# Optimization experiments

Measured on AMD Instinct MI355X. Metric: run time of the kernel, lower is better.

The kernel has to match this reference:

```python
import jax, jax.numpy as jnp
import numpy as np

EPS = 1e-6

def _rms(x, scale):
    # flax nn.RMSNorm: x / sqrt(mean(x^2)+eps) * scale, no mean subtraction
    return x * scale * jax.lax.rsqrt(jnp.mean(x * x, axis=-1, keepdims=True) + EPS)


def _forward(x, mem_k, mem_v, norm1_scale, norm2_scale,
             Wq, bq, Wk, bk, Wv, bv, Wz, bz,
             Wgz, bgz, Wgh, bgh,
             Wg1, bg1, Wg2, bg2, Wgc1, bgc1, Wgc2, bgc2,
             Awq, abq, Awk, abk, Awv, abv, Awo, abo,
             Wf1, bf1, Wf2, bf2):
    B, S, D = x.shape
    M = mem_k.shape[1]
    H = 8
    hd = D // H

    x_norm = _rms(x, norm1_scale)
    q = x_norm @ Wq + bq
    k = x_norm @ Wk + bk
    v = x_norm @ Wv + bv
    z = x_norm @ Wz + bz

    # input-dependent decay gamma in (1e-6, 1-1e-6)
    gamma_base = jax.nn.sigmoid(jax.nn.gelu(z @ Wg1 + bg1) @ Wg2 + bg2)
    gamma_mod = jax.nn.sigmoid(jax.nn.gelu(k @ Wgc1 + bgc1) @ Wgc2 + bgc2)
    gamma = jnp.clip(gamma_base * gamma_mod, 1e-6, 1.0 - 1e-6)

    # gated leaky recurrence over sequence: h depends on W_g_h(h_prev) -> strict scan
    def step(h_prev, zt_gt):
        z_t, g_t = zt_gt  # [B, D] each
        gate = jax.nn.sigmoid(z_t @ Wgz + bgz + h_prev @ Wgh + bgh)
        h_tilde = (1.0 - gate) * h_prev + gate * z_t
        h_t = h_tilde + g_t * h_prev
        return h_t, h_t

    h0 = jnp.zeros((B, D), dtype=x.dtype)
    z_T = jnp.swapaxes(z, 0, 1)          # [S, B, D]
    gamma_T = jnp.swapaxes(gamma, 0, 1)  # [S, B, D]
    _, h_seq_T = jax.lax.scan(step, h0, (z_T, gamma_T))
    h_seq = jnp.swapaxes(h_seq_T, 0, 1)  # [B, S, D]

    # MultiMemoryAttention: q from q_input, K/V from memory state banks [B, M, D]
    qh = (q @ Awq + abq).reshape(B, S, H, hd)
    kh = (mem_k @ Awk + abk).reshape(B, M, H, hd)
    vh = (mem_v @ Awv + abv).reshape(B, M, H, hd)
    scores = jnp.einsum('bshd,bmhd->bhsm', qh, kh) / jnp.sqrt(jnp.asarray(hd, x.dtype))
    probs = jax.nn.softmax(scores, axis=-1)
    mem_out = jnp.einsum('bhsm,bmhd->bshd', probs, vh).reshape(B, S, D) @ Awo + abo

    combined = h_seq + mem_out + v * 0.1
    x_res = x + combined  # dropout deterministic (training=False)

    x_norm2 = _rms(x_res, norm2_scale)
    ffn = jax.nn.gelu(x_norm2 @ Wf1 + bf1) @ Wf2 + bf2
    return x_res + ffn


def setup_inputs() -> dict:
    key = jax.random.key(0)
    B, S, D, H, F, M = 4, 4096, 1024, 8, 4096, 512
    Dq = D // 4
    ks = jax.random.split(key, 24)
    def w(i, shape):
        return jax.random.normal(ks[i], shape, dtype=jnp.float32) * 0.02
    d = {
        'x': jax.random.normal(ks[0], (B, S, D), dtype=jnp.float32),
        'mem_k': jax.random.normal(ks[1], (B, M, D), dtype=jnp.float32),
        'mem_v': jax.random.normal(ks[2], (B, M, D), dtype=jnp.float32),
        'norm1_scale': jnp.ones((D,), jnp.float32),
        'norm2_scale': jnp.ones((D,), jnp.float32),
        'Wq': w(3, (D, D)), 'bq': jnp.zeros((D,), jnp.float32),
        'Wk': w(4, (D, D)), 'bk': jnp.zeros((D,), jnp.float32),
        'Wv': w(5, (D, D)), 'bv': jnp.zeros((D,), jnp.float32),
        'Wz': w(6, (D, D)), 'bz': jnp.zeros((D,), jnp.float32),
        'Wgz': w(7, (D, D)), 'bgz': jnp.zeros((D,), jnp.float32),
        'Wgh': w(8, (D, D)), 'bgh': jnp.zeros((D,), jnp.float32),
        'Wg1': w(9, (D, Dq)), 'bg1': jnp.zeros((Dq,), jnp.float32),
        'Wg2': w(10, (Dq, D)), 'bg2': jnp.zeros((D,), jnp.float32),
        'Wgc1': w(11, (D, Dq)), 'bgc1': jnp.zeros((Dq,), jnp.float32),
        'Wgc2': w(12, (Dq, D)), 'bgc2': jnp.zeros((D,), jnp.float32),
        'Awq': w(13, (D, D)), 'abq': jnp.zeros((D,), jnp.float32),
        'Awk': w(14, (D, D)), 'abk': jnp.zeros((D,), jnp.float32),
        'Awv': w(15, (D, D)), 'abv': jnp.zeros((D,), jnp.float32),
        'Awo': w(16, (D, D)), 'abo': jnp.zeros((D,), jnp.float32),
        'Wf1': w(17, (D, F)), 'bf1': jnp.zeros((F,), jnp.float32),
        'Wf2': w(18, (F, D)), 'bf2': jnp.zeros((D,), jnp.float32),
    }
    return d


def reference(x, mem_k, mem_v, norm1_scale, norm2_scale,
              Wq, bq, Wk, bk, Wv, bv, Wz, bz,
              Wgz, bgz, Wgh, bgh,
              Wg1, bg1, Wg2, bg2, Wgc1, bgc1, Wgc2, bgc2,
              Awq, abq, Awk, abk, Awv, abv, Awo, abo,
              Wf1, bf1, Wf2, bf2):
    return _forward(x, mem_k, mem_v, norm1_scale, norm2_scale,
                    Wq, bq, Wk, bk, Wv, bv, Wz, bz,
                    Wgz, bgz, Wgh, bgh,
                    Wg1, bg1, Wg2, bg2, Wgc1, bgc1, Wgc2, bgc2,
                    Awq, abq, Awk, abk, Awv, abv, Awo, abo,
                    Wf1, bf1, Wf2, bf2)
```

## Files before the change

kernel.cpp:

```cpp
#include <hip/hip_runtime.h>
#include <stdint.h>

typedef short s16x8 __attribute__((ext_vector_type(8)));
typedef float f32x4 __attribute__((ext_vector_type(4)));

#define DEV static __device__ __forceinline__

DEV float bf2f(ushort u){ union{uint i;float f;}v; v.i=((uint)u)<<16; return v.f; }
DEV ushort f2bf(float f){ union{float f;uint i;}v; v.f=f; return (ushort)((v.i + 0x7FFFu + ((v.i>>16)&1u))>>16); }
DEV float fsigmoid(float x){ return 1.f/(1.f+__expf(-x)); }
DEV float fgelu(float x){
  float u = 0.7978845608028654f*(x + 0.044715f*x*x*x);
  float e = __expf(2.f*u);
  float th = 1.f - 2.f/(e+1.f);
  return 0.5f*x*(1.f+th);
}
DEV f32x4 mfma16(s16x8 a, s16x8 b, f32x4 c){
  return __builtin_amdgcn_mfma_f32_16x16x32_bf16(a,b,c,0,0,0);
}

__global__ __launch_bounds__(256) void transpose_cvt(const float* __restrict__ src,
                                                     ushort* __restrict__ dst, int K, int N){
  __shared__ float tile[64][65];
  int tk = blockIdx.y*64, tn = blockIdx.x*64;
  int t = threadIdx.x;
  int c4 = (t & 15)*4, r0 = t >> 4;
  #pragma unroll
  for (int p=0;p<4;++p){
    int r = r0 + p*16;
    float4 v = *(const float4*)(src + (size_t)(tk+r)*N + tn + c4);
    tile[r][c4+0]=v.x; tile[r][c4+1]=v.y; tile[r][c4+2]=v.z; tile[r][c4+3]=v.w;
  }
  __syncthreads();
  #pragma unroll
  for (int p=0;p<4;++p){
    int n = r0 + p*16;
    ushort4 o = make_ushort4(f2bf(tile[c4+0][n]), f2bf(tile[c4+1][n]),
                             f2bf(tile[c4+2][n]), f2bf(tile[c4+3][n]));
    *(ushort4*)(dst + (size_t)(tn+n)*K + tk + c4) = o;
  }
}

__global__ __launch_bounds__(256) void cvt_bf16(const float* __restrict__ s,
                                                ushort* __restrict__ d, int n){
  int i = (blockIdx.x*256 + threadIdx.x)*4;
  if (i < n){
    float4 v = *(const float4*)(s + i);
    ushort4 o = make_ushort4(f2bf(v.x), f2bf(v.y), f2bf(v.z), f2bf(v.w));
    *(ushort4*)(d + i) = o;
  }
}

__global__ __launch_bounds__(256) void bias_sum_k(const float* __restrict__ a,
                                                  const float* __restrict__ b,
                                                  float* __restrict__ o){
  int i = blockIdx.x*256 + threadIdx.x;
  if (i < 1024) o[i] = a[i] + b[i];
}

__global__ __launch_bounds__(256) void fuse_bias(const float* __restrict__ b_in,
                                                 const float* __restrict__ W,
                                                 const float* __restrict__ b_out,
                                                 float* __restrict__ o, int K, int N){
  int n = blockIdx.x*256 + threadIdx.x;
  if (n < N){
    float s = b_out[n];
    for (int k=0;k<K;++k) s += b_in[k]*W[(size_t)k*N + n];
    o[n] = s;
  }
}

__global__ __launch_bounds__(256) void rms_kernel(const float* __restrict__ x,
                                                  const float* __restrict__ scale,
                                                  ushort* __restrict__ out){
  int row = blockIdx.x, t = threadIdx.x;
  const float* xr = x + (size_t)row*1024;
  float4 v = *(const float4*)(xr + t*4);
  float ss = v.x*v.x + v.y*v.y + v.z*v.z + v.w*v.w;
  #pragma unroll
  for (int o=1;o<64;o<<=1) ss += __shfl_xor(ss, o);
  __shared__ float wsum[4];
  if ((t & 63)==0) wsum[t>>6] = ss;
  __syncthreads();
  float tot = wsum[0]+wsum[1]+wsum[2]+wsum[3];
  float rstd = rsqrtf(tot*(1.f/1024.f) + 1e-6f);
  float4 sc = *(const float4*)(scale + t*4);
  ushort4 o4 = make_ushort4(f2bf(v.x*sc.x*rstd), f2bf(v.y*sc.y*rstd),
                            f2bf(v.z*sc.z*rstd), f2bf(v.w*sc.w*rstd));
  *(ushort4*)(out + (size_t)row*1024 + t*4) = o4;
}

template<int EPI>
__global__ __launch_bounds__(256,2) void gemm_bf16(
    const ushort* __restrict__ A, const ushort* __restrict__ Bt,
    const float* __restrict__ bias, void* __restrict__ Cout,
    const void* __restrict__ aux0, const void* __restrict__ aux1,
    int M, int N, int K)
{
  __shared__ ushort Al[128*32];
  __shared__ ushort Bl[128*32];
  const int t = threadIdx.x, ln = t & 63;
  const int m0 = blockIdx.y*128, n0 = blockIdx.x*128;
  const int wv = t >> 6, wr = wv >> 1, wc = wv & 1;
  const int lr = ln & 15, lk = ln >> 4;
  f32x4 acc[4][4] = {};
  for (int kk = 0; kk < K; kk += 32) {
    #pragma unroll
    for (int cc = 0; cc < 2; ++cc) {
      int e = cc*256 + t;
      int r = e >> 2, sg = e & 3;
      s16x8 va = *(const s16x8*)(A  + (size_t)(m0+r)*K + kk + sg*8);
      s16x8 vb = *(const s16x8*)(Bt + (size_t)(n0+r)*K + kk + sg*8);
      *(s16x8*)&Al[e*8] = va;
      *(s16x8*)&Bl[e*8] = vb;
    }
    __syncthreads();
    s16x8 af[4], bfr[4];
    #pragma unroll
    for (int m=0;m<4;++m) af[m]  = *(const s16x8*)&Al[(wr*64 + m*16 + lr)*32 + lk*8];
    #pragma unroll
    for (int n=0;n<4;++n) bfr[n] = *(const s16x8*)&Bl[(wc*64 + n*16 + lr)*32 + lk*8];
    #pragma unroll
    for (int m=0;m<4;++m)
      #pragma unroll
      for (int n=0;n<4;++n)
        acc[m][n] = mfma16(af[m], bfr[n], acc[m][n]);
    __syncthreads();
  }
  #pragma unroll
  for (int m=0;m<4;++m){
    #pragma unroll
    for (int n=0;n<4;++n){
      #pragma unroll
      for (int j=0;j<4;++j){
        int row = m0 + wr*64 + m*16 + lk*4 + j;
        int col = n0 + wc*64 + n*16 + lr;
        float v = acc[m][n][j] + (bias ? bias[col] : 0.f);
        size_t idx = (size_t)row*N + col;
        if constexpr (EPI==0){ ((ushort*)Cout)[idx] = f2bf(v); }
        else if constexpr (EPI==1){ ((ushort*)Cout)[idx] = f2bf(fgelu(v)); }
        else if constexpr (EPI==2){ ((ushort*)Cout)[idx] = f2bf(fsigmoid(v)); }
        else if constexpr (EPI==3){
          float g = fsigmoid(v) * bf2f(((const ushort*)aux0)[idx]);
          g = fminf(fmaxf(g, 1e-6f), 1.f-1e-6f);
          ((ushort*)Cout)[idx] = f2bf(g);
        }
        else if constexpr (EPI==4){
          float o = v + ((const float*)aux0)[idx] + 0.1f*bf2f(((const ushort*)aux1)[idx]);
          ((float*)Cout)[idx] = o;
        }
        else if constexpr (EPI==5){ ((float*)Cout)[idx] += v; }
        else if constexpr (EPI==6){
          int bb = row >> 9, mm = row & 511, hh = col >> 7, dd = col & 127;
          ((ushort*)Cout)[ (((size_t)(bb*8 + hh)*128 + dd) << 9) + mm ] = f2bf(v);
        }
        else if constexpr (EPI==7){
          ((ushort*)Cout)[(size_t)col*M + row] = f2bf(v);
        }
      }
    }
  }
}

__global__ __launch_bounds__(256,1) void attn_kernel(
  const ushort* __restrict__ qh, const ushort* __restrict__ kh,
  const ushort* __restrict__ vhT, ushort* __restrict__ att)
{
  __shared__ ushort P[4*16*512];
  const int t = threadIdx.x, ln = t & 63, wv = t >> 6;
  const int lr = ln & 15, lk = ln >> 4;
  const int b = blockIdx.z, h = blockIdx.y, s0 = blockIdx.x*64;

  const ushort* qrow = qh + (size_t)(b*4096 + s0 + wv*16 + lr)*1024 + h*128 + lk*8;
  s16x8 qf[4];
  #pragma unroll
  for (int kt=0;kt<4;++kt) qf[kt] = *(const s16x8*)(qrow + kt*32);
  __syncthreads();

  f32x4 zero4 = {0.f,0.f,0.f,0.f};
  f32x4 sacc[32];
  #pragma unroll
  for (int i=0;i<32;++i) sacc[i] = zero4;

  const ushort* kbase = kh + (size_t)(b*512)*1024 + h*128 + lk*8;
  #pragma unroll
  for (int mt=0;mt<32;++mt){
    const ushort* krow = kbase + (size_t)(mt*16 + lr)*1024;
    #pragma unroll
    for (int kt=0;kt<4;++kt){
      s16x8 kf = *(const s16x8*)(krow + kt*32);
      sacc[mt] = mfma16(qf[kt], kf, sacc[mt]);
    }
  }
  const float scale = 0.08838834764831845f;
  float inv[4];
  #pragma unroll
  for (int j=0;j<4;++j){
    float m = -3.4e38f;
    #pragma unroll
    for (int mt=0;mt<32;++mt) m = fmaxf(m, sacc[mt][j]);
    m = fmaxf(m, __shfl_xor(m,1)); m = fmaxf(m, __shfl_xor(m,2));
    m = fmaxf(m, __shfl_xor(m,4)); m = fmaxf(m, __shfl_xor(m,8));
    float s = 0.f;
    #pragma unroll
    for (int mt=0;mt<32;++mt){
      float p = __expf((sacc[mt][j]-m)*scale);
      sacc[mt][j] = p; s += p;
    }
    s += __shfl_xor(s,1); s += __shfl_xor(s,2);
    s += __shfl_xor(s,4); s += __shfl_xor(s,8);
    inv[j] = 1.f/s;
  }
  char* pb = (char*)P + wv*16384;
  #pragma unroll
  for (int j=0;j<4;++j){
    int row = lk*4 + j;
    uint xr = (uint)((row & 7) << 4);
    #pragma unroll
    for (int mt=0;mt<32;++mt){
      int col = mt*16 + lr;
      *(ushort*)(pb + row*1024 + (((uint)(col*2)) ^ xr)) = f2bf(sacc[mt][j]);
    }
  }
  f32x4 oacc[8];
  #pragma unroll
  for (int i=0;i<8;++i) oacc[i] = zero4;
  const ushort* vb = vhT + (size_t)(b*8 + h)*128*512;
  const char* prow = (char*)P + wv*16384 + lr*1024;
  uint xrr = (uint)((lr & 7) << 4);
  #pragma unroll
  for (int km=0;km<16;++km){
    s16x8 pf = *(const s16x8*)(prow + (((uint)((km*32 + lk*8)*2)) ^ xrr));
    #pragma unroll
    for (int dt=0;dt<8;++dt){
      s16x8 vf = *(const s16x8*)(vb + (size_t)(dt*16 + lr)*512 + km*32 + lk*8);
      oacc[dt] = mfma16(pf, vf, oacc[dt]);
    }
  }
  ushort* ob = att + (size_t)(b*4096 + s0 + wv*16)*1024 + h*128;
  #pragma unroll
  for (int dt=0;dt<8;++dt){
    #pragma unroll
    for (int j=0;j<4;++j){
      int row = lk*4 + j, col = dt*16 + lr;
      ob[(size_t)row*1024 + col] = f2bf(oacc[dt][j]*inv[j]);
    }
  }
}

#define SCAN_NB 64
__global__ __launch_bounds__(256,1) void scan_kernel(
  const float* __restrict__ Wgh,
  const ushort* __restrict__ u_bf, const ushort* __restrict__ z_bf,
  const ushort* __restrict__ g_bf, float* __restrict__ xres,
  uint* __restrict__ h_buf, unsigned* __restrict__ flags)
{
  __shared__ ushort WL[16*1032];
  __shared__ ushort HL[5*1032];
  __shared__ float  red[4][16][4];
  const int t = threadIdx.x, blk = blockIdx.x;
  const int ln = t & 63, wv = t >> 6;

  {
    const int c = t & 15, i0 = (t >> 4) * 64;
    for (int j = 0; j < 64; ++j) {
      int i = i0 + j;
      WL[c*1032 + i] = f2bf(Wgh[(size_t)i*1024 + blk*16 + c]);
    }
  }
  for (int e = t; e < 1032; e += 256) HL[4*1032 + e] = 0;

  float hmine = 0.f;
  const int c_ep = t & 15, b_ep = t >> 4;
  float uu=0.f, zz=0.f, gg=0.f, xv=0.f;
  if (t < 64) {
    size_t i0 = ((size_t)(b_ep*4096))*1024 + blk*16 + c_ep;
    uu = bf2f(u_bf[i0]); zz = bf2f(z_bf[i0]); gg = bf2f(g_bf[i0]); xv = xres[i0];
  }
  __syncthreads();

  const int arow = ln & 15, akc = ln >> 4;
  const ushort* Abase = &HL[(arow < 4 ? arow : 4)*1032 + akc*8];
  const ushort* Bbase = &WL[(ln & 15)*1032 + akc*8];
  const int hb_t = t >> 6, hk0 = (t & 63)*16;

  for (int step = 0; step < 4096; ++step) {
    if (t < 64) {
      while (__hip_atomic_load(&flags[t*32], __ATOMIC_RELAXED, __HIP_MEMORY_SCOPE_AGENT)
             < (unsigned)step)
        __builtin_amdgcn_s_sleep(1);
    }
    __syncthreads();
    asm volatile("" ::: "memory");
    {
      const uint* hs = h_buf + (size_t)(step & 1)*2048 + hb_t*512 + (hk0 >> 1);
      uint v[8];
      #pragma unroll
      for (int j = 0; j < 8; ++j)
        v[j] = __hip_atomic_load(hs + j, __ATOMIC_RELAXED, __HIP_MEMORY_SCOPE_AGENT);
      uint* dst = (uint*)&HL[hb_t*1032 + hk0];
      *(uint4*)(dst + 0) = make_uint4(v[0], v[1], v[2], v[3]);
      *(uint4*)(dst + 4) = make_uint4(v[4], v[5], v[6], v[7]);
    }
    __syncthreads();
    f32x4 acc = {0.f,0.f,0.f,0.f};
    #pragma unroll
    for (int m = 0; m < 8; ++m) {
      int koff = wv*256 + m*32;
      s16x8 a = *(const s16x8*)(Abase + koff);
      s16x8 b = *(const s16x8*)(Bbase + koff);
      acc = mfma16(a, b, acc);
    }
    if (ln < 16) *(f32x4*)&red[wv][ln][0] = acc;
    __syncthreads();
    if (t < 64) {
      float y = red[0][c_ep][b_ep] + red[1][c_ep][b_ep]
              + red[2][c_ep][b_ep] + red[3][c_ep][b_ep];
      float gate = fsigmoid(y + uu);
      float hn = hmine + gate*(zz - hmine) + gg*hmine;
      hmine = hn;
      int colg = blk*16 + c_ep;
      float hup = __shfl_down(hn, 1);
      if ((t & 1) == 0) {
        uint pk = ((uint)f2bf(hup) << 16) | (uint)f2bf(hn);
        __hip_atomic_store(h_buf + (size_t)((step+1)&1)*2048 + b_ep*512 + (colg>>1), pk,
                           __ATOMIC_RELAXED, __HIP_MEMORY_SCOPE_AGENT);
      }
      size_t idx = ((size_t)(b_ep*4096 + step))*1024 + colg;
      xres[idx] = xv + hn;
      asm volatile("s_waitcnt vmcnt(0)" ::: "memory");
      if (t == 0)
        __hip_atomic_store(&flags[blk*32], (unsigned)(step+1),
                           __ATOMIC_RELAXED, __HIP_MEMORY_SCOPE_AGENT);
      int sn = (step+1 < 4096) ? step+1 : 4095;
      size_t idxn = ((size_t)(b_ep*4096 + sn))*1024 + colg;
      uu = bf2f(u_bf[idxn]); zz = bf2f(z_bf[idxn]); gg = bf2f(g_bf[idxn]);
      xv = xres[idxn];
    }
  }
}

extern "C" void kernel_launch(void* const* d_in, const int* in_sizes, int n_in,
                              void* d_out, int out_size, void* d_ws, size_t ws_size,
                              hipStream_t stream)
{
  const float* x    = (const float*)d_in[0];
  const float* memk = (const float*)d_in[1];
  const float* memv = (const float*)d_in[2];
  const float* n1s  = (const float*)d_in[3];
  const float* n2s  = (const float*)d_in[4];
  const float* Wq = (const float*)d_in[5];   const float* bq = (const float*)d_in[6];
  const float* Wk = (const float*)d_in[7];   const float* bk = (const float*)d_in[8];
  const float* Wv = (const float*)d_in[9];   const float* bv = (const float*)d_in[10];
  const float* Wz = (const float*)d_in[11];  const float* bz = (const float*)d_in[12];
  const float* Wgz = (const float*)d_in[13]; const float* bgz = (const float*)d_in[14];
  const float* Wgh = (const float*)d_in[15]; const float* bgh = (const float*)d_in[16];
  const float* Wg1 = (const float*)d_in[17]; const float* bg1 = (const float*)d_in[18];
  const float* Wg2 = (const float*)d_in[19]; const float* bg2 = (const float*)d_in[20];
  const float* Wgc1 = (const float*)d_in[21]; const float* bgc1 = (const float*)d_in[22];
  const float* Wgc2 = (const float*)d_in[23]; const float* bgc2 = (const float*)d_in[24];
  const float* Awq = (const float*)d_in[25]; const float* abq = (const float*)d_in[26];
  const float* Awk = (const float*)d_in[27]; const float* abk = (const float*)d_in[28];
  const float* Awv = (const float*)d_in[29]; const float* abv = (const float*)d_in[30];
  const float* Awo = (const float*)d_in[31]; const float* abo = (const float*)d_in[32];
  const float* Wf1 = (const float*)d_in[33]; const float* bf1 = (const float*)d_in[34];
  const float* Wf2 = (const float*)d_in[35]; const float* bf2 = (const float*)d_in[36];
  (void)in_sizes; (void)n_in; (void)out_size; (void)ws_size;

  char* ws = (char*)d_ws;
  constexpr size_t MB = 1ull<<20;
  ushort* WvT     = (ushort*)(ws + 0*MB);
  ushort* WzT     = (ushort*)(ws + 2*MB);
  ushort* WgzT    = (ushort*)(ws + 4*MB);
  ushort* WqAwqT  = (ushort*)(ws + 6*MB);
  ushort* AwkT    = (ushort*)(ws + 8*MB);
  ushort* AwvT    = (ushort*)(ws + 10*MB);
  ushort* AwoT    = (ushort*)(ws + 12*MB);
  ushort* Wf1T    = (ushort*)(ws + 14*MB);
  ushort* Wf2Tc   = (ushort*)(ws + 22*MB);
  ushort* Wg1T    = (ushort*)(ws + 30*MB);
  ushort* Wg2T    = (ushort*)(ws + 30*MB + 512*1024);
  ushort* Wgc2T   = (ushort*)(ws + 31*MB);
  ushort* WkWgc1T = (ushort*)(ws + 31*MB + 512*1024);
  float* bsum = (float*)(ws + 32*MB);
  float* bqh  = (float*)(ws + 32*MB + 4096);
  float* bkg  = (float*)(ws + 32*MB + 8192);
  char*  scanB = ws + 32*MB + 65536;
  ushort* Abuf = (ushort*)(ws + 33*MB);
  ushort* Bbuf = (ushort*)(ws + 65*MB);
  ushort* Cbuf = (ushort*)(ws + 97*MB);
  ushort* Dbuf = (ushort*)(ws + 129*MB);
  ushort* Ebuf = (ushort*)(ws + 161*MB);
  char* db = (char*)d_out;
  ushort* t1B   = (ushort*)(db + 0);
  ushort* memkB = (ushort*)(db + 8*MB);
  ushort* memvB = (ushort*)(db + 12*MB);
  ushort* khB   = (ushort*)(db + 16*MB);
  ushort* vhTB  = (ushort*)(db + 20*MB);
  ushort* gbB   = (ushort*)(db + 24*MB);
  ushort* WtmpB = (ushort*)(db + 56*MB);
  ushort* BtTB  = (ushort*)(db + 58*MB);

  const int M1 = 16384;
  dim3 b256(256);
  auto T = [&](const float* s, ushort* d, int K, int N){
    transpose_cvt<<<dim3(N/64, K/64), b256, 0, stream>>>(s, d, K, N);
  };
  #define G(EPI, Ap, Bp, bi, Cp, a0, a1, Mv, Nv, Kv) \
    gemm_bf16<EPI><<<dim3((Nv)/128,(Mv)/128), b256, 0, stream>>>( \
      (const ushort*)(Ap), (const ushort*)(Bp), bi, (void*)(Cp), a0, a1, Mv, Nv, Kv)

  cvt_bf16<<<1024, b256, 0, stream>>>(Wq, WtmpB, 1048576);
  T(Awq, BtTB, 1024, 1024);
  G(7, WtmpB, BtTB, nullptr, WqAwqT, nullptr, nullptr, 1024, 1024, 1024);
  fuse_bias<<<4, b256, 0, stream>>>(bq, Awq, abq, bqh, 1024, 1024);
  cvt_bf16<<<1024, b256, 0, stream>>>(Wk, WtmpB, 1048576);
  T(Wgc1, BtTB, 1024, 256);
  G(7, WtmpB, BtTB, nullptr, WkWgc1T, nullptr, nullptr, 1024, 256, 1024);
  fuse_bias<<<1, b256, 0, stream>>>(bk, Wgc1, bgc1, bkg, 1024, 256);
  T(Wv,WvT,1024,1024); T(Wz,WzT,1024,1024); T(Wgz,WgzT,1024,1024);
  T(Wg1,Wg1T,1024,256); T(Wg2,Wg2T,256,1024); T(Wgc2,Wgc2T,256,1024);
  T(Awk,AwkT,1024,1024); T(Awv,AwvT,1024,1024); T(Awo,AwoT,1024,1024);
  T(Wf1,Wf1T,1024,4096);
  for (int cch = 0; cch < 4; ++cch)
    T(Wf2 + (size_t)cch*1048576, Wf2Tc + (size_t)cch*1048576, 1024, 1024);
  bias_sum_k<<<4, b256, 0, stream>>>(bgz, bgh, bsum);
  cvt_bf16<<<2048, b256, 0, stream>>>(memk, memkB, 2097152);
  cvt_bf16<<<2048, b256, 0, stream>>>(memv, memvB, 2097152);

  rms_kernel<<<M1, b256, 0, stream>>>(x, n1s, Abuf);
  G(0, Abuf, WzT, bz, Bbuf, nullptr, nullptr, M1, 1024, 1024);
  G(0, Abuf, WvT, bv, Cbuf, nullptr, nullptr, M1, 1024, 1024);
  G(0, Abuf, WqAwqT, bqh, Dbuf, nullptr, nullptr, M1, 1024, 1024);
  G(0, Bbuf, WgzT, bsum, Ebuf, nullptr, nullptr, M1, 1024, 1024);
  G(1, Bbuf, Wg1T, bg1, t1B, nullptr, nullptr, M1, 256, 1024);
  G(2, t1B, Wg2T, bg2, gbB, nullptr, nullptr, M1, 1024, 256);
  G(1, Abuf, WkWgc1T, bkg, t1B, nullptr, nullptr, M1, 256, 1024);
  G(3, t1B, Wgc2T, bgc2, Abuf, gbB, nullptr, M1, 1024, 256);
  G(0, memkB, AwkT, abk, khB, nullptr, nullptr, 2048, 1024, 1024);
  G(6, memvB, AwvT, abv, vhTB, nullptr, nullptr, 2048, 1024, 1024);
  attn_kernel<<<dim3(64,8,4), b256, 0, stream>>>(Dbuf, khB, vhTB, Dbuf);
  G(4, Dbuf, AwoT, abo, d_out, (const void*)x, (const void*)Cbuf, M1, 1024, 1024);
  hipMemsetAsync(scanB, 0, 24576, stream);
  scan_kernel<<<SCAN_NB, b256, 0, stream>>>(Wgh, Ebuf, Bbuf, Abuf, (float*)d_out,
                                            (uint*)scanB, (unsigned*)(scanB + 16384));
  rms_kernel<<<M1, b256, 0, stream>>>((const float*)d_out, n2s, Cbuf);
  for (int cch = 0; cch < 4; ++cch) {
    G(1, Cbuf, Wf1T + (size_t)cch*1048576, bf1 + cch*1024, Dbuf, nullptr, nullptr, M1, 1024, 1024);
    G(5, Dbuf, Wf2Tc + (size_t)cch*1048576, (cch==0 ? bf2 : nullptr), d_out, nullptr, nullptr, M1, 1024, 1024);
  }
  #undef G
}
```

Before: 13.07 ms.

## Replace per-block flag barrier with step-tagged 64-bit hidden-state words in scan

```diff
diff --git a/kernel.cpp b/kernel.cpp
--- a/kernel.cpp
+++ b/kernel.cpp
@@ -253,7 +253,7 @@
   const float* __restrict__ Wgh,
   const ushort* __restrict__ u_bf, const ushort* __restrict__ z_bf,
   const ushort* __restrict__ g_bf, float* __restrict__ xres,
-  uint* __restrict__ h_buf, unsigned* __restrict__ flags)
+  unsigned long long* __restrict__ h_buf)
 {
   __shared__ ushort WL[16*1032];
   __shared__ ushort HL[5*1032];
@@ -285,22 +285,26 @@
   const int hb_t = t >> 6, hk0 = (t & 63)*16;
 
   for (int step = 0; step < 4096; ++step) {
-    if (t < 64) {
-      while (__hip_atomic_load(&flags[t*32], __ATOMIC_RELAXED, __HIP_MEMORY_SCOPE_AGENT)
-             < (unsigned)step)
-        __builtin_amdgcn_s_sleep(1);
-    }
-    __syncthreads();
-    asm volatile("" ::: "memory");
     {
-      const uint* hs = h_buf + (size_t)(step & 1)*2048 + hb_t*512 + (hk0 >> 1);
-      uint v[8];
+      const unsigned long long* hs = h_buf + (size_t)(step & 1)*2048 + t*8;
+      unsigned long long v[8];
       #pragma unroll
       for (int j = 0; j < 8; ++j)
         v[j] = __hip_atomic_load(hs + j, __ATOMIC_RELAXED, __HIP_MEMORY_SCOPE_AGENT);
+      while (true) {
+        uint bad = 0;
+        #pragma unroll
+        for (int j = 0; j < 8; ++j)
+          if ((uint)(v[j] >> 32) != (uint)step) bad |= (1u << j);
+        if (!bad) break;
+        #pragma unroll
+        for (int j = 0; j < 8; ++j)
+          if (bad & (1u << j))
+            v[j] = __hip_atomic_load(hs + j, __ATOMIC_RELAXED, __HIP_MEMORY_SCOPE_AGENT);
+      }
       uint* dst = (uint*)&HL[hb_t*1032 + hk0];
-      *(uint4*)(dst + 0) = make_uint4(v[0], v[1], v[2], v[3]);
-      *(uint4*)(dst + 4) = make_uint4(v[4], v[5], v[6], v[7]);
+      *(uint4*)(dst + 0) = make_uint4((uint)v[0], (uint)v[1], (uint)v[2], (uint)v[3]);
+      *(uint4*)(dst + 4) = make_uint4((uint)v[4], (uint)v[5], (uint)v[6], (uint)v[7]);
     }
     __syncthreads();
     f32x4 acc = {0.f,0.f,0.f,0.f};
@@ -322,16 +326,13 @@
       int colg = blk*16 + c_ep;
       float hup = __shfl_down(hn, 1);
       if ((t & 1) == 0) {
-        uint pk = ((uint)f2bf(hup) << 16) | (uint)f2bf(hn);
+        unsigned long long pk = ((unsigned long long)(uint)(step+1) << 32)
+                              | ((uint)f2bf(hup) << 16) | (uint)f2bf(hn);
         __hip_atomic_store(h_buf + (size_t)((step+1)&1)*2048 + b_ep*512 + (colg>>1), pk,
                            __ATOMIC_RELAXED, __HIP_MEMORY_SCOPE_AGENT);
       }
       size_t idx = ((size_t)(b_ep*4096 + step))*1024 + colg;
       xres[idx] = xv + hn;
-      asm volatile("s_waitcnt vmcnt(0)" ::: "memory");
-      if (t == 0)
-        __hip_atomic_store(&flags[blk*32], (unsigned)(step+1),
-                           __ATOMIC_RELAXED, __HIP_MEMORY_SCOPE_AGENT);
       int sn = (step+1 < 4096) ? step+1 : 4095;
       size_t idxn = ((size_t)(b_ep*4096 + sn))*1024 + colg;
       uu = bf2f(u_bf[idxn]); zz = bf2f(z_bf[idxn]); gg = bf2f(g_bf[idxn]);
@@ -441,9 +442,9 @@
   G(6, memvB, AwvT, abv, vhTB, nullptr, nullptr, 2048, 1024, 1024);
   attn_kernel<<<dim3(64,8,4), b256, 0, stream>>>(Dbuf, khB, vhTB, Dbuf);
   G(4, Dbuf, AwoT, abo, d_out, (const void*)x, (const void*)Cbuf, M1, 1024, 1024);
-  hipMemsetAsync(scanB, 0, 24576, stream);
+  hipMemsetAsync(scanB, 0, 32768, stream);
   scan_kernel<<<SCAN_NB, b256, 0, stream>>>(Wgh, Ebuf, Bbuf, Abuf, (float*)d_out,
-                                            (uint*)scanB, (unsigned*)(scanB + 16384));
+                                            (unsigned long long*)scanB);
   rms_kernel<<<M1, b256, 0, stream>>>((const float*)d_out, n2s, Cbuf);
   for (int cch = 0; cch < 4; ++cch) {
     G(1, Cbuf, Wf1T + (size_t)cch*1048576, bf1 + cch*1024, Dbuf, nullptr, nullptr, M1, 1024, 1024);
```

New measurement: 13.31 ms. About the same (+1.8%).
